# Kernel optimization log

Measured on AMD Instinct MI355X. Metric: run time of the kernel, lower is better.

## Reference

```python
import jax, jax.numpy as jnp
import numpy as np

N_NODES = 50000
N_EDGES = 800000
IN_DIM = 128
HID = 32
HEADS = 8
N_CLASSES = 10
N_GRAPHS = 64
NEG_SLOPE = 0.2


def _lin(key, fan_in, fan_out):
    return jax.random.normal(key, (fan_in, fan_out), jnp.float32) / np.sqrt(fan_in)


def setup_inputs() -> dict:
    key = jax.random.key(0)
    ks = jax.random.split(key, 24)
    x = jax.random.normal(ks[0], (N_NODES, IN_DIM), jnp.float32)
    edge_index = jax.random.randint(ks[1], (2, N_EDGES), 0, N_NODES, jnp.int64)
    batch = jnp.sort(jax.random.randint(ks[2], (N_NODES,), 0, N_GRAPHS, jnp.int64))
    HC = HEADS * HID
    return {
        "x": x,
        "edge_index": edge_index,
        "batch": batch,
        # GATConv(IN_DIM, HID, heads=8): shared lin, att_src/att_dst, bias on concat output
        "gat_W": _lin(ks[3], IN_DIM, HC),
        "gat_att_src": jax.random.normal(ks[4], (HEADS, HID), jnp.float32) / np.sqrt(HID),
        "gat_att_dst": jax.random.normal(ks[5], (HEADS, HID), jnp.float32) / np.sqrt(HID),
        "gat_b": jnp.zeros((HC,), jnp.float32),
        # GraphConv(HC, HID): lin_rel (bias) on aggregated neighbors + lin_root (no bias)
        "W2_rel": _lin(ks[6], HC, HID), "b2": jnp.zeros((HID,), jnp.float32), "W2_root": _lin(ks[7], HC, HID),
        # SAGEConv(HID, HID): lin_l (bias) on mean-aggregated neighbors + lin_r (no bias)
        "W3_l": _lin(ks[8], HID, HID), "b3": jnp.zeros((HID,), jnp.float32), "W3_r": _lin(ks[9], HID, HID),
        # GraphConv(HID, HID)
        "W4_rel": _lin(ks[10], HID, HID), "b4": jnp.zeros((HID,), jnp.float32), "W4_root": _lin(ks[11], HID, HID),
        "fc1_W": _lin(ks[12], HID, HID), "fc1_b": jnp.zeros((HID,), jnp.float32),
        "fc2_W": _lin(ks[13], HID, N_CLASSES), "fc2_b": jnp.zeros((N_CLASSES,), jnp.float32),
    }


def _segment_softmax(logits, seg_ids, num_segments):
    # numerically-stable softmax over edges grouped by destination node
    m = jax.ops.segment_max(logits, seg_ids, num_segments=num_segments)
    e = jnp.exp(logits - m[seg_ids])
    z = jax.ops.segment_sum(e, seg_ids, num_segments=num_segments)
    return e / (z[seg_ids] + 1e-16)


def _gnn_forward(x, edge_index, batch, gat_W, gat_att_src, gat_att_dst, gat_b,
                 W2_rel, b2, W2_root, W3_l, b3, W3_r, W4_rel, b4, W4_root,
                 fc1_W, fc1_b, fc2_W, fc2_b):
    N = x.shape[0]
    src0, dst0 = edge_index[0], edge_index[1]

    # ---- GATConv (PyG defaults: add_self_loops=True, concat heads, neg_slope=0.2) ----
    loops = jnp.arange(N)
    src = jnp.concatenate([src0, loops])
    dst = jnp.concatenate([dst0, loops])
    h = (x @ gat_W).reshape(N, HEADS, HID)                 # [N,H,C]
    a_src = jnp.sum(h * gat_att_src, axis=-1)              # [N,H]
    a_dst = jnp.sum(h * gat_att_dst, axis=-1)              # [N,H]
    logits = jax.nn.leaky_relu(a_src[src] + a_dst[dst], NEG_SLOPE)  # [E',H]
    alpha = _segment_softmax(logits, dst, N)               # [E',H]
    msg = h[src] * alpha[:, :, None]                       # [E',H,C]
    out = jax.ops.segment_sum(msg, dst, num_segments=N).reshape(N, HEADS * HID) + gat_b
    x1 = jax.nn.relu(out)

    # ---- GraphConv (aggr='add'): lin_rel(sum_j x_j) + lin_root(x) ----
    agg = jax.ops.segment_sum(x1[src0], dst0, num_segments=N)
    x2 = jax.nn.relu(agg @ W2_rel + b2 + x1 @ W2_root)

    # ---- SAGEConv (aggr='mean'): lin_l(mean_j x_j) + lin_r(x) ----
    deg = jax.ops.segment_sum(jnp.ones((src0.shape[0],), x2.dtype), dst0, num_segments=N)
    agg = jax.ops.segment_sum(x2[src0], dst0, num_segments=N) / jnp.clip(deg, 1.0)[:, None]
    x3 = jax.nn.relu(agg @ W3_l + b3 + x2 @ W3_r)

    # ---- GraphConv ----
    agg = jax.ops.segment_sum(x3[src0], dst0, num_segments=N)
    x4 = jax.nn.relu(agg @ W4_rel + b4 + x3 @ W4_root)

    # ---- global_mean_pool + MLP head ----
    gsum = jax.ops.segment_sum(x4, batch, num_segments=N_GRAPHS)
    gcnt = jax.ops.segment_sum(jnp.ones((N,), x4.dtype), batch, num_segments=N_GRAPHS)
    g = gsum / jnp.clip(gcnt, 1.0)[:, None]                # [G,HID]
    g = jax.nn.relu(g @ fc1_W + fc1_b)
    return g @ fc2_W + fc2_b                               # [G, N_CLASSES]


def reference(x, edge_index, batch, gat_W, gat_att_src, gat_att_dst, gat_b,
              W2_rel, b2, W2_root, W3_l, b3, W3_r, W4_rel, b4, W4_root,
              fc1_W, fc1_b, fc2_W, fc2_b):
    return _gnn_forward(x, edge_index, batch, gat_W, gat_att_src, gat_att_dst, gat_b,
                        W2_rel, b2, W2_root, W3_l, b3, W3_r, W4_rel, b4, W4_root,
                        fc1_W, fc1_b, fc2_W, fc2_b)
```

## Files before the change

### kernel.cpp

```cpp
#include <hip/hip_runtime.h>

#define IN_DIM 128
#define HID 32
#define HEADS 8
#define HC 256
#define N_GRAPHS 64
#define N_CLASSES 10

#define SCAN_ELEMS 8
#define SCAN_BLOCK 256
#define SCAN_CHUNK (SCAN_ELEMS * SCAN_BLOCK)

typedef __attribute__((ext_vector_type(8))) short bf16x8;
typedef __attribute__((ext_vector_type(4))) float f32x4;

__device__ __forceinline__ float leaky(float v) { return v > 0.f ? v : 0.2f * v; }

__device__ __forceinline__ unsigned fenc(float f) {
    unsigned u = __float_as_uint(f);
    return (u & 0x80000000u) ? ~u : (u | 0x80000000u);
}
__device__ __forceinline__ float fdec(unsigned u) {
    return __uint_as_float((u & 0x80000000u) ? (u & 0x7FFFFFFFu) : ~u);
}
__device__ __forceinline__ unsigned short bf16r(float f) {
    unsigned u = __float_as_uint(f);
    return (unsigned short)((u + 0x7FFFu + ((u >> 16) & 1u)) >> 16);
}
__device__ __forceinline__ float bdec(unsigned short u) {
    return __uint_as_float(((unsigned)u) << 16);
}

__global__ __launch_bounds__(256) void k_setup(
    int* __restrict__ deg, int N, unsigned* __restrict__ gm,
    float* __restrict__ gsum, float* __restrict__ gcnt,
    const float* __restrict__ W, const float* __restrict__ Wrel, const float* __restrict__ Wroot,
    unsigned short* __restrict__ Wb, unsigned short* __restrict__ W2b)
{
    int i = blockIdx.x * 256 + threadIdx.x;
    if (i < N) deg[i] = 0;
    if (i < HEADS) gm[i] = 0u;
    if (i < N_GRAPHS * HID) gsum[i] = 0.f;
    if (i < N_GRAPHS) gcnt[i] = 0.f;

    if (blockIdx.x < 16) {
        int slot = blockIdx.x * 256 + threadIdx.x;
        int lane = slot & 63;
        int ctg  = (slot >> 6) & 15;
        int ks   = slot >> 10;
        int col  = ctg * 16 + (lane & 15);
        int kb   = ks * 32 + (lane >> 4) * 8;
        unsigned short t[8];
#pragma unroll
        for (int j = 0; j < 8; ++j) t[j] = bf16r(W[(size_t)(kb + j) * HC + col]);
        ushort4* dst = (ushort4*)(Wb + (size_t)slot * 8);
        dst[0] = make_ushort4(t[0], t[1], t[2], t[3]);
        dst[1] = make_ushort4(t[4], t[5], t[6], t[7]);
    } else if (blockIdx.x < 24) {
        int slot = (blockIdx.x - 16) * 256 + threadIdx.x;
        int lane = slot & 63;
        int ct   = (slot >> 6) & 3;
        int ks   = slot >> 8;
        int col  = ct * 16 + (lane & 15);
        int kb   = ks * 32 + (lane >> 4) * 8;
        const float* src = (col < HID) ? (Wrel + col) : (Wroot + (col - HID));
        unsigned short t[8];
#pragma unroll
        for (int j = 0; j < 8; ++j) t[j] = bf16r(src[(size_t)(kb + j) * HID]);
        ushort4* dst = (ushort4*)(W2b + (size_t)slot * 8);
        dst[0] = make_ushort4(t[0], t[1], t[2], t[3]);
        dst[1] = make_ushort4(t[4], t[5], t[6], t[7]);
    }
}

__global__ __launch_bounds__(256) void k_gemm_deg(
    const float* __restrict__ x, const unsigned short* __restrict__ Wb,
    const float* __restrict__ att_s, const float* __restrict__ att_d,
    unsigned short* __restrict__ h, float* __restrict__ a_src, float* __restrict__ a_dst, int N,
    const int* __restrict__ edst, int* __restrict__ deg, int E, int gemmBlocks)
{
    if (blockIdx.x >= gemmBlocks) {
        int i = (blockIdx.x - gemmBlocks) * 256 + threadIdx.x;
        if (i < E) atomicAdd(&deg[edst[i]], 1);
        return;
    }
    int w = threadIdx.x >> 6;
    int lane = threadIdx.x & 63;
    int lrow = lane & 15, lgrp = lane >> 4;
    int nb = blockIdx.x * 16;

    int rowc = min(nb + lrow, N - 1);
    const float* xrow = x + (size_t)rowc * IN_DIM + lgrp * 8;

    f32x4 acc0 = {0.f, 0.f, 0.f, 0.f}, acc1 = acc0, acc2 = acc0, acc3 = acc0;

#pragma unroll
    for (int ks = 0; ks < 4; ++ks) {
        float4 a0 = *(const float4*)(xrow + ks * 32);
        float4 a1 = *(const float4*)(xrow + ks * 32 + 4);
        bf16x8 af;
        af[0] = (short)bf16r(a0.x); af[1] = (short)bf16r(a0.y);
        af[2] = (short)bf16r(a0.z); af[3] = (short)bf16r(a0.w);
        af[4] = (short)bf16r(a1.x); af[5] = (short)bf16r(a1.y);
        af[6] = (short)bf16r(a1.z); af[7] = (short)bf16r(a1.w);
        const bf16x8* bp = (const bf16x8*)(Wb + ((size_t)(ks * 16 + w * 4) * 64 + lane) * 8);
        acc0 = __builtin_amdgcn_mfma_f32_16x16x32_bf16(af, bp[0 * 64], acc0, 0, 0, 0);
        acc1 = __builtin_amdgcn_mfma_f32_16x16x32_bf16(af, bp[1 * 64], acc1, 0, 0, 0);
        acc2 = __builtin_amdgcn_mfma_f32_16x16x32_bf16(af, bp[2 * 64], acc2, 0, 0, 0);
        acc3 = __builtin_amdgcn_mfma_f32_16x16x32_bf16(af, bp[3 * 64], acc3, 0, 0, 0);
    }

    int cbase = w * 64;
#pragma unroll
    for (int r = 0; r < 4; ++r) {
        int n = nb + lgrp * 4 + r;
        if (n < N) {
            unsigned short* hp = h + (size_t)n * HC + cbase + lrow;
            hp[0]  = bf16r(acc0[r]);
            hp[16] = bf16r(acc1[r]);
            hp[32] = bf16r(acc2[r]);
            hp[48] = bf16r(acc3[r]);
        }
    }
    int h0 = cbase >> 5, h1 = h0 + 1;
    float as00 = att_s[h0 * HID + lrow], as01 = att_s[h0 * HID + 16 + lrow];
    float as10 = att_s[h1 * HID + lrow], as11 = att_s[h1 * HID + 16 + lrow];
    float ad00 = att_d[h0 * HID + lrow], ad01 = att_d[h0 * HID + 16 + lrow];
    float ad10 = att_d[h1 * HID + lrow], ad11 = att_d[h1 * HID + 16 + lrow];
#pragma unroll
    for (int r = 0; r < 4; ++r) {
        float ps0 = acc0[r] * as00 + acc1[r] * as01;
        float pd0 = acc0[r] * ad00 + acc1[r] * ad01;
        float ps1 = acc2[r] * as10 + acc3[r] * as11;
        float pd1 = acc2[r] * ad10 + acc3[r] * ad11;
#pragma unroll
        for (int d = 1; d < 16; d <<= 1) {
            ps0 += __shfl_xor(ps0, d); pd0 += __shfl_xor(pd0, d);
            ps1 += __shfl_xor(ps1, d); pd1 += __shfl_xor(pd1, d);
        }
        int n = nb + lgrp * 4 + r;
        if (lrow == 0 && n < N) {
            a_src[n * HEADS + h0] = ps0; a_dst[n * HEADS + h0] = pd0;
            a_src[n * HEADS + h1] = ps1; a_dst[n * HEADS + h1] = pd1;
        }
    }
}

__global__ __launch_bounds__(256) void k_amax_scan(
    const float* __restrict__ asrc, unsigned* __restrict__ gm, int N,
    const int* __restrict__ deg, int* __restrict__ bsum, int amaxBlocks)
{
    int tid = threadIdx.x;
    if (blockIdx.x < amaxBlocks) {
        __shared__ float sm[4][HEADS];
        float m[HEADS];
#pragma unroll
        for (int hh = 0; hh < HEADS; ++hh) m[hh] = -1e30f;
        int stride = amaxBlocks * 256;
        for (int n = blockIdx.x * 256 + tid; n < N; n += stride) {
#pragma unroll
            for (int hh = 0; hh < HEADS; ++hh) m[hh] = fmaxf(m[hh], asrc[n * HEADS + hh]);
        }
#pragma unroll
        for (int hh = 0; hh < HEADS; ++hh)
            for (int d = 1; d < 64; d <<= 1) m[hh] = fmaxf(m[hh], __shfl_xor(m[hh], d));
        int lane = tid & 63, wv = tid >> 6;
        if (lane == 0)
#pragma unroll
            for (int hh = 0; hh < HEADS; ++hh) sm[wv][hh] = m[hh];
        __syncthreads();
        if (tid == 0) {
#pragma unroll
            for (int hh = 0; hh < HEADS; ++hh) {
                float mm = fmaxf(fmaxf(sm[0][hh], sm[1][hh]), fmaxf(sm[2][hh], sm[3][hh]));
                atomicMax(&gm[hh], fenc(mm));
            }
        }
    } else {
        int bid = blockIdx.x - amaxBlocks;
        int base = bid * SCAN_CHUNK + tid * SCAN_ELEMS;
        int s = 0;
#pragma unroll
        for (int i = 0; i < SCAN_ELEMS; ++i) { int idx = base + i; if (idx < N) s += deg[idx]; }
#pragma unroll
        for (int d = 1; d < 64; d <<= 1) s += __shfl_xor(s, d);
        __shared__ int ws[4];
        int lane = tid & 63, wv = tid >> 6;
        if (lane == 0) ws[wv] = s;
        __syncthreads();
        if (tid == 0) bsum[bid] = ws[0] + ws[1] + ws[2] + ws[3];
    }
}

__global__ __launch_bounds__(64) void k_scan_bsum(int* __restrict__ bsum, int nb,
                                                  int* __restrict__ total_out)
{
    int lane = threadIdx.x;
    int v = (lane < nb) ? bsum[lane] : 0;
    int orig = v;
#pragma unroll
    for (int d = 1; d < 64; d <<= 1) { int t = __shfl_up(v, d); if (lane >= d) v += t; }
    if (lane < nb) bsum[lane] = v - orig;
    if (lane == nb - 1) *total_out = v;
}

__global__ __launch_bounds__(SCAN_BLOCK) void k_scan_write(
    const int* __restrict__ deg, const int* __restrict__ bsum,
    int* __restrict__ off, int* __restrict__ cursor, int N)
{
    int base = blockIdx.x * SCAN_CHUNK + threadIdx.x * SCAN_ELEMS;
    int dl[SCAN_ELEMS];
    int s = 0;
#pragma unroll
    for (int i = 0; i < SCAN_ELEMS; ++i) {
        int idx = base + i;
        dl[i] = (idx < N) ? deg[idx] : 0;
        s += dl[i];
    }
    int lane = threadIdx.x & 63, wv = threadIdx.x >> 6;
    int v = s;
#pragma unroll
    for (int d = 1; d < 64; d <<= 1) { int t = __shfl_up(v, d); if (lane >= d) v += t; }
    __shared__ int ws[4];
    if (lane == 63) ws[wv] = v;
    __syncthreads();
    int wadd = 0;
    for (int w = 0; w < wv; ++w) wadd += ws[w];
    int run = bsum[blockIdx.x] + wadd + (v - s);
#pragma unroll
    for (int i = 0; i < SCAN_ELEMS; ++i) {
        int idx = base + i;
        if (idx < N) { off[idx] = run; cursor[idx] = run; run += dl[i]; }
    }
}

__global__ void k_scatter(const int* __restrict__ src, const int* __restrict__ dst,
                          int* __restrict__ cursor, unsigned short* __restrict__ srcs, int E) {
    int i = blockIdx.x * blockDim.x + threadIdx.x;
    if (i < E) { int p = atomicAdd(&cursor[dst[i]], 1); srcs[p] = (unsigned short)src[i]; }
}

__global__ __launch_bounds__(256) void k_gat(
    const unsigned short* __restrict__ h, const float* __restrict__ asrc, const float* __restrict__ adst,
    const float* __restrict__ bias, const int* __restrict__ off, const unsigned short* __restrict__ srcs,
    const unsigned* __restrict__ gm, unsigned short* __restrict__ x1, int N)
{
    int v = (blockIdx.x * blockDim.x + threadIdx.x) >> 6;
    int lane = threadIdx.x & 63;
    if (v >= N) return;
    int head = lane >> 3;
    float ad = adst[v * HEADS + head];
    float asv = asrc[v * HEADS + head];
    float m = leaky(fdec(gm[head]) + ad);
    int beg = off[v], end = off[v + 1];

    ushort4 hv = *(const ushort4*)(h + (size_t)v * HC + lane * 4);
    float w = __expf(leaky(asv + ad) - m);
    float z = w;
    float acc0 = w * bdec(hv.x), acc1 = w * bdec(hv.y), acc2 = w * bdec(hv.z), acc3 = w * bdec(hv.w);

    int e = beg;
    for (; e + 4 <= end; e += 4) {
        int s0 = srcs[e + 0], s1 = srcs[e + 1], s2 = srcs[e + 2], s3 = srcs[e + 3];
        float l0 = asrc[s0 * HEADS + head], l1 = asrc[s1 * HEADS + head];
        float l2 = asrc[s2 * HEADS + head], l3 = asrc[s3 * HEADS + head];
        ushort4 h0 = *(const ushort4*)(h + (size_t)s0 * HC + lane * 4);
        ushort4 h1 = *(const ushort4*)(h + (size_t)s1 * HC + lane * 4);
        ushort4 h2 = *(const ushort4*)(h + (size_t)s2 * HC + lane * 4);
        ushort4 h3 = *(const ushort4*)(h + (size_t)s3 * HC + lane * 4);
        float w0 = __expf(leaky(l0 + ad) - m);
        float w1 = __expf(leaky(l1 + ad) - m);
        float w2 = __expf(leaky(l2 + ad) - m);
        float w3 = __expf(leaky(l3 + ad) - m);
        z += (w0 + w1) + (w2 + w3);
        acc0 += w0 * bdec(h0.x) + w1 * bdec(h1.x) + w2 * bdec(h2.x) + w3 * bdec(h3.x);
        acc1 += w0 * bdec(h0.y) + w1 * bdec(h1.y) + w2 * bdec(h2.y) + w3 * bdec(h3.y);
        acc2 += w0 * bdec(h0.z) + w1 * bdec(h1.z) + w2 * bdec(h2.z) + w3 * bdec(h3.z);
        acc3 += w0 * bdec(h0.w) + w1 * bdec(h1.w) + w2 * bdec(h2.w) + w3 * bdec(h3.w);
    }
    for (; e < end; ++e) {
        int s = srcs[e];
        float we = __expf(leaky(asrc[s * HEADS + head] + ad) - m);
        ushort4 hs = *(const ushort4*)(h + (size_t)s * HC + lane * 4);
        z += we;
        acc0 += we * bdec(hs.x); acc1 += we * bdec(hs.y);
        acc2 += we * bdec(hs.z); acc3 += we * bdec(hs.w);
    }
    float inv_z = 1.f / (z + 1e-16f);
    int c = lane * 4;
    float4 b4 = *(const float4*)(bias + c);
    ushort4 o;
    o.x = bf16r(fmaxf(acc0 * inv_z + b4.x, 0.f));
    o.y = bf16r(fmaxf(acc1 * inv_z + b4.y, 0.f));
    o.z = bf16r(fmaxf(acc2 * inv_z + b4.z, 0.f));
    o.w = bf16r(fmaxf(acc3 * inv_z + b4.w, 0.f));
    *(ushort4*)(x1 + (size_t)v * HC + c) = o;
}

__global__ __launch_bounds__(256) void k_zr2(
    const unsigned short* __restrict__ x1b, const unsigned short* __restrict__ W2b,
    unsigned short* __restrict__ z, float* __restrict__ r, int N)
{
    int w = threadIdx.x >> 6;
    int lane = threadIdx.x & 63;
    int lrow = lane & 15, lgrp = lane >> 4;
    int nb = blockIdx.x * 16;
    int rowc = min(nb + lrow, N - 1);
    const unsigned short* xrow = x1b + (size_t)rowc * HC + lgrp * 8;

    f32x4 acc = {0.f, 0.f, 0.f, 0.f};
#pragma unroll
    for (int ks = 0; ks < 8; ++ks) {
        bf16x8 af = *(const bf16x8*)(xrow + ks * 32);
        const bf16x8* bp = (const bf16x8*)(W2b + ((size_t)(ks * 4 + w) * 64 + lane) * 8);
        acc = __builtin_amdgcn_mfma_f32_16x16x32_bf16(af, *bp, acc, 0, 0, 0);
    }
    int col = w * 16 + lrow;
#pragma unroll
    for (int rr = 0; rr < 4; ++rr) {
        int n = nb + lgrp * 4 + rr;
        if (n < N) {
            if (col < HID) z[(size_t)n * HID + col] = bf16r(acc[rr]);
            else           r[(size_t)n * HID + (col - HID)] = acc[rr];
        }
    }
}

__global__ __launch_bounds__(256) void k_agg_lin(
    const unsigned short* __restrict__ z, const float* __restrict__ r, const float* __restrict__ b,
    const int* __restrict__ off, const unsigned short* __restrict__ srcs,
    unsigned short* __restrict__ xout, int N)
{
    int nl = threadIdx.x >> 5, j = threadIdx.x & 31;
    int n = blockIdx.x * 8 + nl;
    if (n >= N) return;
    float acc = r[n * HID + j] + b[j];
    int beg = off[n], end = off[n + 1];
    int e = beg;
    for (; e + 4 <= end; e += 4) {
        int s0 = srcs[e], s1 = srcs[e + 1], s2 = srcs[e + 2], s3 = srcs[e + 3];
        float v0 = bdec(z[s0 * HID + j]);
        float v1 = bdec(z[s1 * HID + j]);
        float v2 = bdec(z[s2 * HID + j]);
        float v3 = bdec(z[s3 * HID + j]);
        acc += (v0 + v1) + (v2 + v3);
    }
    for (; e < end; ++e)
        acc += bdec(z[srcs[e] * HID + j]);
    xout[n * HID + j] = bf16r(fmaxf(acc, 0.f));
}

template <bool MEAN>
__global__ __launch_bounds__(256) void k_conv32(
    const unsigned short* __restrict__ xin, const int* __restrict__ off, const unsigned short* __restrict__ srcs,
    const float* __restrict__ Wl, const float* __restrict__ Wr, const float* __restrict__ b,
    unsigned short* __restrict__ xout, int N)
{
    __shared__ float sagg[8][HID];
    __shared__ float sx[8][HID];
    int nl = threadIdx.x >> 5, j = threadIdx.x & 31;
    int n = blockIdx.x * 8 + nl;
    int nc = min(n, N - 1);
    int beg = off[nc], end = off[nc + 1];
    float acc = 0.f;
    int e = beg;
    for (; e + 4 <= end; e += 4) {
        int s0 = srcs[e], s1 = srcs[e + 1], s2 = srcs[e + 2], s3 = srcs[e + 3];
        float v0 = bdec(xin[s0 * HID + j]);
        float v1 = bdec(xin[s1 * HID + j]);
        float v2 = bdec(xin[s2 * HID + j]);
        float v3 = bdec(xin[s3 * HID + j]);
        acc += (v0 + v1) + (v2 + v3);
    }
    for (; e < end; ++e)
        acc += bdec(xin[srcs[e] * HID + j]);
    if (MEAN) acc /= fmaxf((float)(end - beg), 1.f);
    sagg[nl][j] = acc;
    sx[nl][j] = bdec(xin[nc * HID + j]);
    __syncthreads();
    float o = b[j];
#pragma unroll
    for (int k = 0; k < HID; ++k)
        o += sagg[nl][k] * Wl[k * HID + j] + sx[nl][k] * Wr[k * HID + j];
    o = fmaxf(o, 0.f);
    if (n < N) xout[n * HID + j] = bf16r(o);
}

__global__ __launch_bounds__(256) void k_pool(
    const unsigned short* __restrict__ x4, const int* __restrict__ batch,
    float* __restrict__ gsum, float* __restrict__ gcnt, int N)
{
    const int PER_BLOCK = 1024;
    int base = blockIdx.x * PER_BLOCK;
    int endn = min(base + PER_BLOCK, N);
    int c = threadIdx.x & 31, no = threadIdx.x >> 5;
    float acc = 0.f, cnt = 0.f;
    int curg = -1;
    for (int n = base + no; n < endn; n += 8) {
        int g = batch[n];
        if (g != curg) {
            if (curg >= 0) {
                atomicAdd(&gsum[curg * HID + c], acc);
                if (c == 0) atomicAdd(&gcnt[curg], cnt);
            }
            curg = g; acc = 0.f; cnt = 0.f;
        }
        acc += bdec(x4[n * HID + c]);
        cnt += 1.f;
    }
    if (curg >= 0) {
        atomicAdd(&gsum[curg * HID + c], acc);
        if (c == 0) atomicAdd(&gcnt[curg], cnt);
    }
}

__global__ __launch_bounds__(1024) void k_head(
    const float* __restrict__ gsum, const float* __restrict__ gcnt,
    const float* __restrict__ fc1W, const float* __restrict__ fc1b,
    const float* __restrict__ fc2W, const float* __restrict__ fc2b,
    float* __restrict__ out)
{
    __shared__ float g[N_GRAPHS * HID];
    __shared__ float t[N_GRAPHS * HID];
    int tid = threadIdx.x;
    for (int i = tid; i < N_GRAPHS * HID; i += 1024) {
        int gi = i >> 5;
        g[i] = gsum[i] / fmaxf(gcnt[gi], 1.f);
    }
    __syncthreads();
    for (int i = tid; i < N_GRAPHS * HID; i += 1024) {
        int gi = i >> 5, j = i & 31;
        float o = fc1b[j];
#pragma unroll
        for (int k = 0; k < HID; ++k) o += g[gi * HID + k] * fc1W[k * HID + j];
        t[i] = fmaxf(o, 0.f);
    }
    __syncthreads();
    for (int i = tid; i < N_GRAPHS * N_CLASSES; i += 1024) {
        int gi = i / N_CLASSES, j = i % N_CLASSES;
        float o = fc2b[j];
#pragma unroll
        for (int k = 0; k < HID; ++k) o += t[gi * HID + k] * fc2W[k * N_CLASSES + j];
        out[i] = o;
    }
}

extern "C" void kernel_launch(void* const* d_in, const int* in_sizes, int n_in,
                              void* d_out, int out_size, void* d_ws, size_t ws_size,
                              hipStream_t stream)
{
    const float* x       = (const float*)d_in[0];
    const int*   eidx    = (const int*)d_in[1];
    const int*   batch   = (const int*)d_in[2];
    const float* gat_W   = (const float*)d_in[3];
    const float* att_s   = (const float*)d_in[4];
    const float* att_d   = (const float*)d_in[5];
    const float* gat_b   = (const float*)d_in[6];
    const float* W2_rel  = (const float*)d_in[7];
    const float* b2      = (const float*)d_in[8];
    const float* W2_root = (const float*)d_in[9];
    const float* W3_l    = (const float*)d_in[10];
    const float* b3      = (const float*)d_in[11];
    const float* W3_r    = (const float*)d_in[12];
    const float* W4_rel  = (const float*)d_in[13];
    const float* b4      = (const float*)d_in[14];
    const float* W4_root = (const float*)d_in[15];
    const float* fc1_W   = (const float*)d_in[16];
    const float* fc1_b   = (const float*)d_in[17];
    const float* fc2_W   = (const float*)d_in[18];
    const float* fc2_b   = (const float*)d_in[19];

    const int N = in_sizes[2];
    const int E = in_sizes[1] / 2;
    const int* esrc = eidx;
    const int* edst = eidx + E;

    char* wsb = (char*)d_ws;
    size_t ofs = 0;
    auto alloc = [&](size_t bytes) {
        char* p = wsb + ofs;
        ofs = (ofs + bytes + 255) & ~(size_t)255;
        return p;
    };
    unsigned short* h   = (unsigned short*)alloc((size_t)N * HC * 2);
    unsigned short* Wb  = (unsigned short*)alloc((size_t)IN_DIM * HC * 2);
    unsigned short* W2b = (unsigned short*)alloc((size_t)HC * 64 * 2);
    unsigned short* x1b = (unsigned short*)alloc((size_t)N * HC * 2);
    float* a_src = (float*)alloc((size_t)N * HEADS * 4);
    float* a_dst = (float*)alloc((size_t)N * HEADS * 4);
    int*   deg   = (int*)alloc((size_t)N * 4);
    int*   off   = (int*)alloc((size_t)(N + 1) * 4);
    int*   cur   = (int*)alloc((size_t)N * 4);
    unsigned short* srcs = (unsigned short*)alloc((size_t)E * 2);
    int*   bsum  = (int*)alloc((size_t)128 * 4);
    unsigned short* zb  = (unsigned short*)alloc((size_t)N * HID * 2);
    float* r     = (float*)alloc((size_t)N * HID * 4);
    unsigned short* x2b = (unsigned short*)alloc((size_t)N * HID * 2);
    unsigned short* x3b = (unsigned short*)alloc((size_t)N * HID * 2);
    unsigned short* x4b = (unsigned short*)alloc((size_t)N * HID * 2);
    float* gsum  = (float*)alloc(N_GRAPHS * HID * 4);
    float* gcnt  = (float*)alloc(N_GRAPHS * 4);
    unsigned* gm = (unsigned*)alloc(HEADS * 4);
    (void)ws_size; (void)n_in; (void)out_size;

    const int nscan = (N + SCAN_CHUNK - 1) / SCAN_CHUNK;
    const int gemmBlocks = (N + 15) / 16;
    const int degBlocks  = (E + 255) / 256;
    const int amaxBlocks = 32;

    k_setup<<<(N + 255) / 256, 256, 0, stream>>>(deg, N, gm, gsum, gcnt,
                                                 gat_W, W2_rel, W2_root, Wb, W2b);
    k_gemm_deg<<<gemmBlocks + degBlocks, 256, 0, stream>>>(
        x, Wb, att_s, att_d, h, a_src, a_dst, N, edst, deg, E, gemmBlocks);
    k_amax_scan<<<amaxBlocks + nscan, 256, 0, stream>>>(a_src, gm, N, deg, bsum, amaxBlocks);
    k_scan_bsum<<<1, 64, 0, stream>>>(bsum, nscan, off + N);
    k_scan_write<<<nscan, SCAN_BLOCK, 0, stream>>>(deg, bsum, off, cur, N);
    k_scatter<<<(E + 255) / 256, 256, 0, stream>>>(esrc, edst, cur, srcs, E);
    k_gat<<<(N + 3) / 4, 256, 0, stream>>>(h, a_src, a_dst, gat_b, off, srcs, gm, x1b, N);
    k_zr2<<<(N + 15) / 16, 256, 0, stream>>>(x1b, W2b, zb, r, N);
    k_agg_lin<<<(N + 7) / 8, 256, 0, stream>>>(zb, r, b2, off, srcs, x2b, N);
    k_conv32<true><<<(N + 7) / 8, 256, 0, stream>>>(x2b, off, srcs, W3_l, W3_r, b3, x3b, N);
    k_conv32<false><<<(N + 7) / 8, 256, 0, stream>>>(x3b, off, srcs, W4_rel, W4_root, b4, x4b, N);
    k_pool<<<(N + 1023) / 1024, 256, 0, stream>>>(x4b, batch, gsum, gcnt, N);
    k_head<<<1, 1024, 0, stream>>>(gsum, gcnt, fc1_W, fc1_b, fc2_W, fc2_b, (float*)d_out);
}
```

Measured before the change: 336.9 us.

## Record per-edge rank at degree count, drop scatter atomics and merge small kernels

The degree-count pass now stores each edge's atomic return value as a rank, so the scatter writes to off[dst]+rank directly instead of performing a second atomic on a cursor array. The single-block bsum scan kernel is removed; each scan_write block serially sums the preceding block totals itself. Pool and head are fused with a last-block-done counter, so the MLP head runs in the final pool block. The aim is fewer launches and fewer atomics, at the cost of an extra rank array (16-bit, so it assumes node degree stays below 65536) and a serial prefix loop per block.

```diff
diff --git a/kernel.cpp b/kernel.cpp
--- a/kernel.cpp
+++ b/kernel.cpp
@@ -33,7 +33,7 @@
 
 __global__ __launch_bounds__(256) void k_setup(
     int* __restrict__ deg, int N, unsigned* __restrict__ gm,
-    float* __restrict__ gsum, float* __restrict__ gcnt,
+    float* __restrict__ gsum, float* __restrict__ gcnt, int* __restrict__ counter,
     const float* __restrict__ W, const float* __restrict__ Wrel, const float* __restrict__ Wroot,
     unsigned short* __restrict__ Wb, unsigned short* __restrict__ W2b)
 {
@@ -42,6 +42,7 @@
     if (i < HEADS) gm[i] = 0u;
     if (i < N_GRAPHS * HID) gsum[i] = 0.f;
     if (i < N_GRAPHS) gcnt[i] = 0.f;
+    if (i == 0) *counter = 0;
 
     if (blockIdx.x < 16) {
         int slot = blockIdx.x * 256 + threadIdx.x;
@@ -77,11 +78,12 @@
     const float* __restrict__ x, const unsigned short* __restrict__ Wb,
     const float* __restrict__ att_s, const float* __restrict__ att_d,
     unsigned short* __restrict__ h, float* __restrict__ a_src, float* __restrict__ a_dst, int N,
-    const int* __restrict__ edst, int* __restrict__ deg, int E, int gemmBlocks)
+    const int* __restrict__ edst, int* __restrict__ deg, unsigned short* __restrict__ rank,
+    int E, int gemmBlocks)
 {
     if (blockIdx.x >= gemmBlocks) {
         int i = (blockIdx.x - gemmBlocks) * 256 + threadIdx.x;
-        if (i < E) atomicAdd(&deg[edst[i]], 1);
+        if (i < E) rank[i] = (unsigned short)atomicAdd(&deg[edst[i]], 1);
         return;
     }
     int w = threadIdx.x >> 6;
@@ -192,22 +194,16 @@
     }
 }
 
-__global__ __launch_bounds__(64) void k_scan_bsum(int* __restrict__ bsum, int nb,
-                                                  int* __restrict__ total_out)
-{
-    int lane = threadIdx.x;
-    int v = (lane < nb) ? bsum[lane] : 0;
-    int orig = v;
-#pragma unroll
-    for (int d = 1; d < 64; d <<= 1) { int t = __shfl_up(v, d); if (lane >= d) v += t; }
-    if (lane < nb) bsum[lane] = v - orig;
-    if (lane == nb - 1) *total_out = v;
-}
-
 __global__ __launch_bounds__(SCAN_BLOCK) void k_scan_write(
     const int* __restrict__ deg, const int* __restrict__ bsum,
-    int* __restrict__ off, int* __restrict__ cursor, int N)
-{
+    int* __restrict__ off, int N)
+{
+    __shared__ int sbpre;
+    if (threadIdx.x == 0) {
+        int s = 0;
+        for (int b = 0; b < blockIdx.x; ++b) s += bsum[b];
+        sbpre = s;
+    }
     int base = blockIdx.x * SCAN_CHUNK + threadIdx.x * SCAN_ELEMS;
     int dl[SCAN_ELEMS];
     int s = 0;
@@ -226,18 +222,23 @@
     __syncthreads();
     int wadd = 0;
     for (int w = 0; w < wv; ++w) wadd += ws[w];
-    int run = bsum[blockIdx.x] + wadd + (v - s);
+    int run = sbpre + wadd + (v - s);
 #pragma unroll
     for (int i = 0; i < SCAN_ELEMS; ++i) {
         int idx = base + i;
-        if (idx < N) { off[idx] = run; cursor[idx] = run; run += dl[i]; }
+        if (idx < N) {
+            off[idx] = run;
+            run += dl[i];
+            if (idx == N - 1) off[N] = run;
+        }
     }
 }
 
 __global__ void k_scatter(const int* __restrict__ src, const int* __restrict__ dst,
-                          int* __restrict__ cursor, unsigned short* __restrict__ srcs, int E) {
+                          const unsigned short* __restrict__ rank, const int* __restrict__ off,
+                          unsigned short* __restrict__ srcs, int E) {
     int i = blockIdx.x * blockDim.x + threadIdx.x;
-    if (i < E) { int p = atomicAdd(&cursor[dst[i]], 1); srcs[p] = (unsigned short)src[i]; }
+    if (i < E) srcs[off[dst[i]] + (int)rank[i]] = (unsigned short)src[i];
 }
 
 __global__ __launch_bounds__(256) void k_gat(
@@ -386,49 +387,53 @@
     if (n < N) xout[n * HID + j] = bf16r(o);
 }
 
-__global__ __launch_bounds__(256) void k_pool(
+__global__ __launch_bounds__(256) void k_pool_head(
     const unsigned short* __restrict__ x4, const int* __restrict__ batch,
-    float* __restrict__ gsum, float* __restrict__ gcnt, int N)
+    float* __restrict__ gsum, float* __restrict__ gcnt, int N, int* __restrict__ counter,
+    const float* __restrict__ fc1W, const float* __restrict__ fc1b,
+    const float* __restrict__ fc2W, const float* __restrict__ fc2b,
+    float* __restrict__ out)
 {
     const int PER_BLOCK = 1024;
     int base = blockIdx.x * PER_BLOCK;
     int endn = min(base + PER_BLOCK, N);
     int c = threadIdx.x & 31, no = threadIdx.x >> 5;
-    float acc = 0.f, cnt = 0.f;
-    int curg = -1;
-    for (int n = base + no; n < endn; n += 8) {
-        int g = batch[n];
-        if (g != curg) {
-            if (curg >= 0) {
-                atomicAdd(&gsum[curg * HID + c], acc);
-                if (c == 0) atomicAdd(&gcnt[curg], cnt);
+    {
+        float acc = 0.f, cnt = 0.f;
+        int curg = -1;
+        for (int n = base + no; n < endn; n += 8) {
+            int g = batch[n];
+            if (g != curg) {
+                if (curg >= 0) {
+                    atomicAdd(&gsum[curg * HID + c], acc);
+                    if (c == 0) atomicAdd(&gcnt[curg], cnt);
+                }
+                curg = g; acc = 0.f; cnt = 0.f;
             }
-            curg = g; acc = 0.f; cnt = 0.f;
-        }
-        acc += bdec(x4[n * HID + c]);
-        cnt += 1.f;
-    }
-    if (curg >= 0) {
-        atomicAdd(&gsum[curg * HID + c], acc);
-        if (c == 0) atomicAdd(&gcnt[curg], cnt);
-    }
-}
-
-__global__ __launch_bounds__(1024) void k_head(
-    const float* __restrict__ gsum, const float* __restrict__ gcnt,
-    const float* __restrict__ fc1W, const float* __restrict__ fc1b,
-    const float* __restrict__ fc2W, const float* __restrict__ fc2b,
-    float* __restrict__ out)
-{
+            acc += bdec(x4[n * HID + c]);
+            cnt += 1.f;
+        }
+        if (curg >= 0) {
+            atomicAdd(&gsum[curg * HID + c], acc);
+            if (c == 0) atomicAdd(&gcnt[curg], cnt);
+        }
+    }
+    __threadfence();
+    __shared__ int lastFlag;
+    if (threadIdx.x == 0) lastFlag = (atomicAdd(counter, 1) == (int)gridDim.x - 1);
+    __syncthreads();
+    if (!lastFlag) return;
+
     __shared__ float g[N_GRAPHS * HID];
     __shared__ float t[N_GRAPHS * HID];
+    __shared__ float gc[N_GRAPHS];
     int tid = threadIdx.x;
-    for (int i = tid; i < N_GRAPHS * HID; i += 1024) {
-        int gi = i >> 5;
-        g[i] = gsum[i] / fmaxf(gcnt[gi], 1.f);
-    }
+    if (tid < N_GRAPHS) gc[tid] = atomicAdd(&gcnt[tid], 0.f);
     __syncthreads();
-    for (int i = tid; i < N_GRAPHS * HID; i += 1024) {
+    for (int i = tid; i < N_GRAPHS * HID; i += 256)
+        g[i] = atomicAdd(&gsum[i], 0.f) / fmaxf(gc[i >> 5], 1.f);
+    __syncthreads();
+    for (int i = tid; i < N_GRAPHS * HID; i += 256) {
         int gi = i >> 5, j = i & 31;
         float o = fc1b[j];
 #pragma unroll
@@ -436,7 +441,7 @@
         t[i] = fmaxf(o, 0.f);
     }
     __syncthreads();
-    for (int i = tid; i < N_GRAPHS * N_CLASSES; i += 1024) {
+    for (int i = tid; i < N_GRAPHS * N_CLASSES; i += 256) {
         int gi = i / N_CLASSES, j = i % N_CLASSES;
         float o = fc2b[j];
 #pragma unroll
@@ -490,7 +495,7 @@
     float* a_dst = (float*)alloc((size_t)N * HEADS * 4);
     int*   deg   = (int*)alloc((size_t)N * 4);
     int*   off   = (int*)alloc((size_t)(N + 1) * 4);
-    int*   cur   = (int*)alloc((size_t)N * 4);
+    unsigned short* rank = (unsigned short*)alloc((size_t)E * 2);
     unsigned short* srcs = (unsigned short*)alloc((size_t)E * 2);
     int*   bsum  = (int*)alloc((size_t)128 * 4);
     unsigned short* zb  = (unsigned short*)alloc((size_t)N * HID * 2);
@@ -501,26 +506,27 @@
     float* gsum  = (float*)alloc(N_GRAPHS * HID * 4);
     float* gcnt  = (float*)alloc(N_GRAPHS * 4);
     unsigned* gm = (unsigned*)alloc(HEADS * 4);
+    int*  counter = (int*)alloc(4);
     (void)ws_size; (void)n_in; (void)out_size;
 
     const int nscan = (N + SCAN_CHUNK - 1) / SCAN_CHUNK;
     const int gemmBlocks = (N + 15) / 16;
     const int degBlocks  = (E + 255) / 256;
     const int amaxBlocks = 32;
-
-    k_setup<<<(N + 255) / 256, 256, 0, stream>>>(deg, N, gm, gsum, gcnt,
+    const int poolBlocks = (N + 1023) / 1024;
+
+    k_setup<<<(N + 255) / 256, 256, 0, stream>>>(deg, N, gm, gsum, gcnt, counter,
                                                  gat_W, W2_rel, W2_root, Wb, W2b);
     k_gemm_deg<<<gemmBlocks + degBlocks, 256, 0, stream>>>(
-        x, Wb, att_s, att_d, h, a_src, a_dst, N, edst, deg, E, gemmBlocks);
+        x, Wb, att_s, att_d, h, a_src, a_dst, N, edst, deg, rank, E, gemmBlocks);
     k_amax_scan<<<amaxBlocks + nscan, 256, 0, stream>>>(a_src, gm, N, deg, bsum, amaxBlocks);
-    k_scan_bsum<<<1, 64, 0, stream>>>(bsum, nscan, off + N);
-    k_scan_write<<<nscan, SCAN_BLOCK, 0, stream>>>(deg, bsum, off, cur, N);
-    k_scatter<<<(E + 255) / 256, 256, 0, stream>>>(esrc, edst, cur, srcs, E);
+    k_scan_write<<<nscan, SCAN_BLOCK, 0, stream>>>(deg, bsum, off, N);
+    k_scatter<<<(E + 255) / 256, 256, 0, stream>>>(esrc, edst, rank, off, srcs, E);
     k_gat<<<(N + 3) / 4, 256, 0, stream>>>(h, a_src, a_dst, gat_b, off, srcs, gm, x1b, N);
     k_zr2<<<(N + 15) / 16, 256, 0, stream>>>(x1b, W2b, zb, r, N);
     k_agg_lin<<<(N + 7) / 8, 256, 0, stream>>>(zb, r, b2, off, srcs, x2b, N);
     k_conv32<true><<<(N + 7) / 8, 256, 0, stream>>>(x2b, off, srcs, W3_l, W3_r, b3, x3b, N);
     k_conv32<false><<<(N + 7) / 8, 256, 0, stream>>>(x3b, off, srcs, W4_rel, W4_root, b4, x4b, N);
-    k_pool<<<(N + 1023) / 1024, 256, 0, stream>>>(x4b, batch, gsum, gcnt, N);
-    k_head<<<1, 1024, 0, stream>>>(gsum, gcnt, fc1_W, fc1_b, fc2_W, fc2_b, (float*)d_out);
-}
+    k_pool_head<<<poolBlocks, 256, 0, stream>>>(x4b, batch, gsum, gcnt, N, counter,
+                                                fc1_W, fc1_b, fc2_W, fc2_b, (float*)d_out);
+}
```

Result: faster. 309.2 us (-8.2%).
